# Performance work log

Measured on AMD Instinct MI355X. Metric: run time of the kernel, lower is better.

The kernel has to match this reference:

```python
import jax, jax.numpy as jnp
import numpy as np

RBF_START = 0.0
RBF_END = 12.0
RBF_STEPS = 32
ENERGY_SCALE = 0.01


def setup_inputs() -> dict:
    key = jax.random.key(0)
    k1, k2, k3, k4 = jax.random.split(key, 4)
    B, L, R, E, F = 8, 128, 2048, RBF_STEPS, 64
    return {
        "lig_feat": jax.random.normal(k1, (B, L, E, F), dtype=jnp.float32),
        "rec_feat": jax.random.normal(k2, (B, R, E, F), dtype=jnp.float32),
        "lig_coord": jax.random.normal(k3, (B, L, 3), dtype=jnp.float32),
        "rec_coord": jax.random.normal(k4, (B, R, 3), dtype=jnp.float32),
    }


def reference(lig_feat, rec_feat, lig_coord, rec_coord):
    # atn_coefs: contract feature dim f -> [B, L, R, E]
    atn_coefs = jnp.einsum('blef,bref->blre', lig_feat, rec_feat)
    # pairwise distances [B, L, R]
    diff = lig_coord[:, :, None, :] - rec_coord[:, None, :, :]
    dists = jnp.sqrt(jnp.sum(diff * diff, axis=-1))
    # RBF expansion [B, L, R, E]
    mu = jnp.linspace(RBF_START, RBF_END, RBF_STEPS, dtype=jnp.float32)
    sigma = (RBF_START - RBF_END) / RBF_STEPS
    z = (dists[..., None] - mu) / sigma
    rbfs = jnp.exp(-(z * z))
    # per-entry scalar energy [B]
    U = jnp.sum(atn_coefs * rbfs * ENERGY_SCALE, axis=(1, 2, 3))
    return U
```

## Files before the change

kernel.cpp:

```cpp
#include <hip/hip_runtime.h>
#include <hip/hip_bf16.h>

#define NB 8
#define NL 128
#define NR 2048
#define NE 32
#define NF 64
#define RT 128
#define NRT (NR / RT)
#define EH 4
#define EPB (NE / EH)
#define NTHREADS 512
#define NWAVES (NTHREADS / 64)

typedef __attribute__((ext_vector_type(4)))  float f32x4;
typedef __attribute__((ext_vector_type(16))) float f32x16;
typedef __attribute__((ext_vector_type(8)))  short s16x8;

__device__ __forceinline__ unsigned short f2bf(float x) {
    union { float f; unsigned u; } v; v.f = x;
    unsigned u = v.u;
    u += 0x7fffu + ((u >> 16) & 1u);
    return (unsigned short)(u >> 16);
}

__device__ __forceinline__ unsigned long long pack4(f32x4 v) {
    unsigned long long lo = (unsigned)f2bf(v.x) | ((unsigned)f2bf(v.y) << 16);
    unsigned long long hi = (unsigned)f2bf(v.z) | ((unsigned)f2bf(v.w) << 16);
    return lo | (hi << 32);
}

__global__ __launch_bounds__(NTHREADS, 4) void ff_kernel(
    const float* __restrict__ lig_feat,
    const float* __restrict__ rec_feat,
    const float* __restrict__ lig_coord,
    const float* __restrict__ rec_coord,
    float* __restrict__ out)
{
    __shared__ __align__(16) unsigned short sA[2][NL * NF];
    __shared__ __align__(16) unsigned short sB[2][RT * NF];
    __shared__ float sLc[3][NL];
    __shared__ float sRc[3][RT];
    __shared__ float sRed[NWAVES];

    const int blk = blockIdx.x;
    const int eh  = blk & (EH - 1);
    const int rt  = (blk >> 2) & (NRT - 1);
    const int b   = blk >> 6;
    const int e0  = eh * EPB;
    const int r0  = rt * RT;
    const int t   = threadIdx.x;
    const int lane = t & 63;
    const int wv   = t >> 6;

    for (int i = t; i < 3 * NL; i += NTHREADS) {
        const int c = i >> 7, l = i & 127;
        sLc[c][l] = lig_coord[((long)b * NL + l) * 3 + c];
    }
    for (int i = t; i < 3 * RT; i += NTHREADS) {
        const int c = i >> 7, r = i & 127;
        sRc[c][r] = rec_coord[((long)b * NR + r0 + r) * 3 + c];
    }

    f32x4 tA[4], tB[4];
    #pragma unroll
    for (int j = 0; j < 4; ++j) {
        const int idx = t + NTHREADS * j;
        const int f4 = idx & 15, l = idx >> 4;
        tA[j] = *(const f32x4*)(lig_feat + (((long)b * NL + l) * NE + e0) * NF + f4 * 4);
    }
    #pragma unroll
    for (int j = 0; j < 4; ++j) {
        const int idx = t + NTHREADS * j;
        const int f4 = idx & 15, r = idx >> 4;
        tB[j] = *(const f32x4*)(rec_feat + (((long)b * NR + r0 + r) * NE + e0) * NF + f4 * 4);
    }
    __syncthreads();

    const int n  = lane & 31;
    const int h  = lane >> 5;
    const int tr  = wv & 3;
    const int tl0 = wv >> 2;
    const int colr = tr * 32 + n;
    const float rx = sRc[0][colr], ry = sRc[1][colr], rz = sRc[2][colr];
    float d[2][16];
    #pragma unroll
    for (int t2 = 0; t2 < 2; ++t2) {
        const int tl = tl0 + 2 * t2;
        #pragma unroll
        for (int i = 0; i < 16; ++i) {
            const int row = tl * 32 + 4 * h + (i & 3) + ((i >> 2) << 3);
            const float dx = sLc[0][row] - rx;
            const float dy = sLc[1][row] - ry;
            const float dz = sLc[2][row] - rz;
            d[t2][i] = sqrtf(dx * dx + dy * dy + dz * dz);
        }
    }

    #pragma unroll
    for (int j = 0; j < 4; ++j) {
        const int idx = t + NTHREADS * j;
        const int f4 = idx & 15, l = idx >> 4;
        const int pos = (((f4 >> 1) ^ (l & 7)) << 3) + ((f4 & 1) << 2);
        *(unsigned long long*)&sA[0][l * NF + pos] = pack4(tA[j]);
    }
    #pragma unroll
    for (int j = 0; j < 4; ++j) {
        const int idx = t + NTHREADS * j;
        const int f4 = idx & 15, r = idx >> 4;
        const int pos = (((f4 >> 1) ^ (r & 7)) << 3) + ((f4 & 1) << 2);
        *(unsigned long long*)&sB[0][r * NF + pos] = pack4(tB[j]);
    }
    if (EPB > 1) {
        #pragma unroll
        for (int j = 0; j < 4; ++j) {
            const int idx = t + NTHREADS * j;
            const int f4 = idx & 15, l = idx >> 4;
            tA[j] = *(const f32x4*)(lig_feat + (((long)b * NL + l) * NE + e0 + 1) * NF + f4 * 4);
        }
        #pragma unroll
        for (int j = 0; j < 4; ++j) {
            const int idx = t + NTHREADS * j;
            const int f4 = idx & 15, r = idx >> 4;
            tB[j] = *(const f32x4*)(rec_feat + (((long)b * NR + r0 + r) * NE + e0 + 1) * NF + f4 * 4);
        }
    }
    __syncthreads();

    const float inv_s   = 32.0f / 12.0f;
    const float mu_step = 12.0f / 31.0f;
    const int sw = (n & 7);
    const int aBase = (tl0 * 32 + n) * NF;
    const int bBase = (tr * 32 + n) * NF;

    float sum = 0.0f;

    for (int ep = 0; ep < EPB; ++ep) {
        const int cur = ep & 1;

        if (ep + 1 < EPB) {
            #pragma unroll
            for (int j = 0; j < 4; ++j) {
                const int idx = t + NTHREADS * j;
                const int f4 = idx & 15, l = idx >> 4;
                const int pos = (((f4 >> 1) ^ (l & 7)) << 3) + ((f4 & 1) << 2);
                *(unsigned long long*)&sA[cur ^ 1][l * NF + pos] = pack4(tA[j]);
            }
            #pragma unroll
            for (int j = 0; j < 4; ++j) {
                const int idx = t + NTHREADS * j;
                const int f4 = idx & 15, r = idx >> 4;
                const int pos = (((f4 >> 1) ^ (r & 7)) << 3) + ((f4 & 1) << 2);
                *(unsigned long long*)&sB[cur ^ 1][r * NF + pos] = pack4(tB[j]);
            }
        }
        if (ep + 2 < EPB) {
            const int en = e0 + ep + 2;
            #pragma unroll
            for (int j = 0; j < 4; ++j) {
                const int idx = t + NTHREADS * j;
                const int f4 = idx & 15, l = idx >> 4;
                tA[j] = *(const f32x4*)(lig_feat + (((long)b * NL + l) * NE + en) * NF + f4 * 4);
            }
            #pragma unroll
            for (int j = 0; j < 4; ++j) {
                const int idx = t + NTHREADS * j;
                const int f4 = idx & 15, r = idx >> 4;
                tB[j] = *(const f32x4*)(rec_feat + (((long)b * NR + r0 + r) * NE + en) * NF + f4 * 4);
            }
        }

        const float mu = (float)(e0 + ep) * mu_step;
        #pragma unroll
        for (int t2 = 0; t2 < 2; ++t2) {
            const unsigned short* pa = &sA[cur][aBase + t2 * 64 * NF];
            const unsigned short* pb = &sB[cur][bBase];
            f32x16 acc = {0,0,0,0,0,0,0,0,0,0,0,0,0,0,0,0};
            #pragma unroll
            for (int kc = 0; kc < 4; ++kc) {
                const int ck = kc * 2 + h;
                const s16x8 af = *(const s16x8*)&pa[(ck ^ sw) << 3];
                const s16x8 bf = *(const s16x8*)&pb[(ck ^ sw) << 3];
                acc = __builtin_amdgcn_mfma_f32_32x32x16_bf16(af, bf, acc, 0, 0, 0);
            }
            #pragma unroll
            for (int i = 0; i < 16; ++i) {
                const float z = (d[t2][i] - mu) * inv_s;
                sum += __expf(-z * z) * acc[i];
            }
        }

        if (ep + 1 < EPB) __syncthreads();
    }

    sum *= 0.01f;
    #pragma unroll
    for (int off = 32; off > 0; off >>= 1)
        sum += __shfl_down(sum, off, 64);
    if (lane == 0) sRed[wv] = sum;
    __syncthreads();
    if (t == 0) {
        float s = 0.f;
        #pragma unroll
        for (int w = 0; w < NWAVES; ++w) s += sRed[w];
        atomicAdd(&out[b], s);
    }
}

extern "C" void kernel_launch(void* const* d_in, const int* in_sizes, int n_in,
                              void* d_out, int out_size, void* d_ws, size_t ws_size,
                              hipStream_t stream) {
    const float* lig_feat  = (const float*)d_in[0];
    const float* rec_feat  = (const float*)d_in[1];
    const float* lig_coord = (const float*)d_in[2];
    const float* rec_coord = (const float*)d_in[3];
    float* out = (float*)d_out;

    hipMemsetAsync(out, 0, (size_t)out_size * sizeof(float), stream);

    dim3 grid(NB * NRT * EH);
    ff_kernel<<<grid, NTHREADS, 0, stream>>>(lig_feat, rec_feat,
                                             lig_coord, rec_coord, out);
}
```

Before: 207.7 us.

## Use 2x2 MFMA tiles per wave with 256 threads and cheaper bf16 packing

Halves the block to 256 threads and gives each wave a 64x64 output tile computed as a 2x2 grid of 32x32 MFMAs, so every LDS fragment feeds two MFMAs instead of one. bf16 conversion now uses a single perm with round-half-up instead of round-to-nearest-even bit arithmetic, and the RBF argument becomes one fma with a precomputed negative mu. This cuts LDS read traffic and ALU work per MFMA, but raises register use (more staging registers and four accumulators), and the launch bound drops to 2 blocks, which may lower occupancy.

```diff
diff --git a/kernel.cpp b/kernel.cpp
--- a/kernel.cpp
+++ b/kernel.cpp
@@ -10,27 +10,27 @@
 #define NRT (NR / RT)
 #define EH 4
 #define EPB (NE / EH)
-#define NTHREADS 512
+#define NTHREADS 256
 #define NWAVES (NTHREADS / 64)
 
 typedef __attribute__((ext_vector_type(4)))  float f32x4;
 typedef __attribute__((ext_vector_type(16))) float f32x16;
 typedef __attribute__((ext_vector_type(8)))  short s16x8;
-
-__device__ __forceinline__ unsigned short f2bf(float x) {
-    union { float f; unsigned u; } v; v.f = x;
-    unsigned u = v.u;
-    u += 0x7fffu + ((u >> 16) & 1u);
-    return (unsigned short)(u >> 16);
-}
-
-__device__ __forceinline__ unsigned long long pack4(f32x4 v) {
-    unsigned long long lo = (unsigned)f2bf(v.x) | ((unsigned)f2bf(v.y) << 16);
-    unsigned long long hi = (unsigned)f2bf(v.z) | ((unsigned)f2bf(v.w) << 16);
-    return lo | (hi << 32);
-}
-
-__global__ __launch_bounds__(NTHREADS, 4) void ff_kernel(
+typedef __attribute__((ext_vector_type(2)))  unsigned int u32x2;
+
+__device__ __forceinline__ unsigned bf16pair(float a, float b) {
+    union { float f; unsigned u; } ua, ub; ua.f = a; ub.f = b;
+    return __builtin_amdgcn_perm(ub.u + 0x8000u, ua.u + 0x8000u, 0x07060302u);
+}
+
+__device__ __forceinline__ u32x2 pack4(f32x4 v) {
+    u32x2 r;
+    r.x = bf16pair(v.x, v.y);
+    r.y = bf16pair(v.z, v.w);
+    return r;
+}
+
+__global__ __launch_bounds__(NTHREADS, 2) void ff_kernel(
     const float* __restrict__ lig_feat,
     const float* __restrict__ rec_feat,
     const float* __restrict__ lig_coord,
@@ -62,15 +62,15 @@
         sRc[c][r] = rec_coord[((long)b * NR + r0 + r) * 3 + c];
     }
 
-    f32x4 tA[4], tB[4];
-    #pragma unroll
-    for (int j = 0; j < 4; ++j) {
+    f32x4 tA[8], tB[8];
+    #pragma unroll
+    for (int j = 0; j < 8; ++j) {
         const int idx = t + NTHREADS * j;
         const int f4 = idx & 15, l = idx >> 4;
         tA[j] = *(const f32x4*)(lig_feat + (((long)b * NL + l) * NE + e0) * NF + f4 * 4);
     }
     #pragma unroll
-    for (int j = 0; j < 4; ++j) {
+    for (int j = 0; j < 8; ++j) {
         const int idx = t + NTHREADS * j;
         const int f4 = idx & 15, r = idx >> 4;
         tB[j] = *(const f32x4*)(rec_feat + (((long)b * NR + r0 + r) * NE + e0) * NF + f4 * 4);
@@ -79,47 +79,49 @@
 
     const int n  = lane & 31;
     const int h  = lane >> 5;
-    const int tr  = wv & 3;
-    const int tl0 = wv >> 2;
-    const int colr = tr * 32 + n;
-    const float rx = sRc[0][colr], ry = sRc[1][colr], rz = sRc[2][colr];
-    float d[2][16];
-    #pragma unroll
-    for (int t2 = 0; t2 < 2; ++t2) {
-        const int tl = tl0 + 2 * t2;
-        #pragma unroll
-        for (int i = 0; i < 16; ++i) {
-            const int row = tl * 32 + 4 * h + (i & 3) + ((i >> 2) << 3);
-            const float dx = sLc[0][row] - rx;
-            const float dy = sLc[1][row] - ry;
-            const float dz = sLc[2][row] - rz;
-            d[t2][i] = sqrtf(dx * dx + dy * dy + dz * dz);
-        }
-    }
-
-    #pragma unroll
-    for (int j = 0; j < 4; ++j) {
+    const int wl = wv >> 1;
+    const int wr = wv & 1;
+    float d[2][2][16];
+    #pragma unroll
+    for (int j2 = 0; j2 < 2; ++j2) {
+        const int col = wr * 64 + j2 * 32 + n;
+        const float rx = sRc[0][col], ry = sRc[1][col], rz = sRc[2][col];
+        #pragma unroll
+        for (int i2 = 0; i2 < 2; ++i2) {
+            #pragma unroll
+            for (int i = 0; i < 16; ++i) {
+                const int row = wl * 64 + i2 * 32 + 4 * h + (i & 3) + ((i >> 2) << 3);
+                const float dx = sLc[0][row] - rx;
+                const float dy = sLc[1][row] - ry;
+                const float dz = sLc[2][row] - rz;
+                d[i2][j2][i] = sqrtf(dx * dx + dy * dy + dz * dz);
+            }
+        }
+    }
+
+    #pragma unroll
+    for (int j = 0; j < 8; ++j) {
         const int idx = t + NTHREADS * j;
         const int f4 = idx & 15, l = idx >> 4;
         const int pos = (((f4 >> 1) ^ (l & 7)) << 3) + ((f4 & 1) << 2);
-        *(unsigned long long*)&sA[0][l * NF + pos] = pack4(tA[j]);
-    }
-    #pragma unroll
-    for (int j = 0; j < 4; ++j) {
+        *(u32x2*)&sA[0][l * NF + pos] = pack4(tA[j]);
+    }
+    #pragma unroll
+    for (int j = 0; j < 8; ++j) {
         const int idx = t + NTHREADS * j;
         const int f4 = idx & 15, r = idx >> 4;
         const int pos = (((f4 >> 1) ^ (r & 7)) << 3) + ((f4 & 1) << 2);
-        *(unsigned long long*)&sB[0][r * NF + pos] = pack4(tB[j]);
+        *(u32x2*)&sB[0][r * NF + pos] = pack4(tB[j]);
     }
     if (EPB > 1) {
         #pragma unroll
-        for (int j = 0; j < 4; ++j) {
+        for (int j = 0; j < 8; ++j) {
             const int idx = t + NTHREADS * j;
             const int f4 = idx & 15, l = idx >> 4;
             tA[j] = *(const f32x4*)(lig_feat + (((long)b * NL + l) * NE + e0 + 1) * NF + f4 * 4);
         }
         #pragma unroll
-        for (int j = 0; j < 4; ++j) {
+        for (int j = 0; j < 8; ++j) {
             const int idx = t + NTHREADS * j;
             const int f4 = idx & 15, r = idx >> 4;
             tB[j] = *(const f32x4*)(rec_feat + (((long)b * NR + r0 + r) * NE + e0 + 1) * NF + f4 * 4);
@@ -128,10 +130,9 @@
     __syncthreads();
 
     const float inv_s   = 32.0f / 12.0f;
-    const float mu_step = 12.0f / 31.0f;
     const int sw = (n & 7);
-    const int aBase = (tl0 * 32 + n) * NF;
-    const int bBase = (tr * 32 + n) * NF;
+    const int aRow0 = (wl * 64 + n) * NF;
+    const int bRow0 = (wr * 64 + n) * NF;
 
     float sum = 0.0f;
 
@@ -140,54 +141,58 @@
 
         if (ep + 1 < EPB) {
             #pragma unroll
-            for (int j = 0; j < 4; ++j) {
+            for (int j = 0; j < 8; ++j) {
                 const int idx = t + NTHREADS * j;
                 const int f4 = idx & 15, l = idx >> 4;
                 const int pos = (((f4 >> 1) ^ (l & 7)) << 3) + ((f4 & 1) << 2);
-                *(unsigned long long*)&sA[cur ^ 1][l * NF + pos] = pack4(tA[j]);
-            }
-            #pragma unroll
-            for (int j = 0; j < 4; ++j) {
+                *(u32x2*)&sA[cur ^ 1][l * NF + pos] = pack4(tA[j]);
+            }
+            #pragma unroll
+            for (int j = 0; j < 8; ++j) {
                 const int idx = t + NTHREADS * j;
                 const int f4 = idx & 15, r = idx >> 4;
                 const int pos = (((f4 >> 1) ^ (r & 7)) << 3) + ((f4 & 1) << 2);
-                *(unsigned long long*)&sB[cur ^ 1][r * NF + pos] = pack4(tB[j]);
+                *(u32x2*)&sB[cur ^ 1][r * NF + pos] = pack4(tB[j]);
             }
         }
         if (ep + 2 < EPB) {
             const int en = e0 + ep + 2;
             #pragma unroll
-            for (int j = 0; j < 4; ++j) {
+            for (int j = 0; j < 8; ++j) {
                 const int idx = t + NTHREADS * j;
                 const int f4 = idx & 15, l = idx >> 4;
                 tA[j] = *(const f32x4*)(lig_feat + (((long)b * NL + l) * NE + en) * NF + f4 * 4);
             }
             #pragma unroll
-            for (int j = 0; j < 4; ++j) {
+            for (int j = 0; j < 8; ++j) {
                 const int idx = t + NTHREADS * j;
                 const int f4 = idx & 15, r = idx >> 4;
                 tB[j] = *(const f32x4*)(rec_feat + (((long)b * NR + r0 + r) * NE + en) * NF + f4 * 4);
             }
         }
 
-        const float mu = (float)(e0 + ep) * mu_step;
-        #pragma unroll
-        for (int t2 = 0; t2 < 2; ++t2) {
-            const unsigned short* pa = &sA[cur][aBase + t2 * 64 * NF];
-            const unsigned short* pb = &sB[cur][bBase];
-            f32x16 acc = {0,0,0,0,0,0,0,0,0,0,0,0,0,0,0,0};
-            #pragma unroll
-            for (int kc = 0; kc < 4; ++kc) {
-                const int ck = kc * 2 + h;
-                const s16x8 af = *(const s16x8*)&pa[(ck ^ sw) << 3];
-                const s16x8 bf = *(const s16x8*)&pb[(ck ^ sw) << 3];
-                acc = __builtin_amdgcn_mfma_f32_32x32x16_bf16(af, bf, acc, 0, 0, 0);
-            }
-            #pragma unroll
-            for (int i = 0; i < 16; ++i) {
-                const float z = (d[t2][i] - mu) * inv_s;
-                sum += __expf(-z * z) * acc[i];
-            }
+        f32x16 acc00 = {0,0,0,0,0,0,0,0,0,0,0,0,0,0,0,0};
+        f32x16 acc01 = acc00, acc10 = acc00, acc11 = acc00;
+        #pragma unroll
+        for (int kc = 0; kc < 4; ++kc) {
+            const int off = (((kc * 2 + h) ^ sw) << 3);
+            const s16x8 a0 = *(const s16x8*)&sA[cur][aRow0 + off];
+            const s16x8 a1 = *(const s16x8*)&sA[cur][aRow0 + 32 * NF + off];
+            const s16x8 b0 = *(const s16x8*)&sB[cur][bRow0 + off];
+            const s16x8 b1 = *(const s16x8*)&sB[cur][bRow0 + 32 * NF + off];
+            acc00 = __builtin_amdgcn_mfma_f32_32x32x16_bf16(a0, b0, acc00, 0, 0, 0);
+            acc01 = __builtin_amdgcn_mfma_f32_32x32x16_bf16(a0, b1, acc01, 0, 0, 0);
+            acc10 = __builtin_amdgcn_mfma_f32_32x32x16_bf16(a1, b0, acc10, 0, 0, 0);
+            acc11 = __builtin_amdgcn_mfma_f32_32x32x16_bf16(a1, b1, acc11, 0, 0, 0);
+        }
+        const float nmu = -(float)(e0 + ep) * (32.0f / 31.0f);
+        #pragma unroll
+        for (int i = 0; i < 16; ++i) {
+            float z;
+            z = __builtin_fmaf(d[0][0][i], inv_s, nmu); sum += __expf(-z * z) * acc00[i];
+            z = __builtin_fmaf(d[0][1][i], inv_s, nmu); sum += __expf(-z * z) * acc01[i];
+            z = __builtin_fmaf(d[1][0][i], inv_s, nmu); sum += __expf(-z * z) * acc10[i];
+            z = __builtin_fmaf(d[1][1][i], inv_s, nmu); sum += __expf(-z * z) * acc11[i];
         }
 
         if (ep + 1 < EPB) __syncthreads();
```

Result: slower. 223.2 us (+7.5%).

## Pipeline feature loads with inline-asm async loads and interleaved dual MFMA tiles

Applied to the files above, without the earlier changes.

Global feature loads become inline-asm global_load_dwordx4 with an explicit s_waitcnt placed after the MFMA and RBF work, so the prefetch for step ep+2 overlaps compute. The two MFMA accumulator chains are interleaved and share B-fragment loads. The bf16 pack uses a cheaper round-half-up conversion with v_perm, and the RBF argument is computed as a single fma. Launch bounds drop to 2 blocks per CU to allow more registers, which may reduce occupancy. The bf16 rounding no longer uses ties-to-even.

```diff
diff --git a/kernel.cpp b/kernel.cpp
--- a/kernel.cpp
+++ b/kernel.cpp
@@ -1,5 +1,4 @@
 #include <hip/hip_runtime.h>
-#include <hip/hip_bf16.h>
 
 #define NB 8
 #define NL 128
@@ -16,21 +15,25 @@
 typedef __attribute__((ext_vector_type(4)))  float f32x4;
 typedef __attribute__((ext_vector_type(16))) float f32x16;
 typedef __attribute__((ext_vector_type(8)))  short s16x8;
-
-__device__ __forceinline__ unsigned short f2bf(float x) {
-    union { float f; unsigned u; } v; v.f = x;
-    unsigned u = v.u;
-    u += 0x7fffu + ((u >> 16) & 1u);
-    return (unsigned short)(u >> 16);
-}
-
-__device__ __forceinline__ unsigned long long pack4(f32x4 v) {
-    unsigned long long lo = (unsigned)f2bf(v.x) | ((unsigned)f2bf(v.y) << 16);
-    unsigned long long hi = (unsigned)f2bf(v.z) | ((unsigned)f2bf(v.w) << 16);
-    return lo | (hi << 32);
-}
-
-__global__ __launch_bounds__(NTHREADS, 4) void ff_kernel(
+typedef __attribute__((ext_vector_type(2)))  unsigned int u32x2;
+
+__device__ __forceinline__ unsigned bf16pair(float a, float b) {
+    union { float f; unsigned u; } ua, ub; ua.f = a; ub.f = b;
+    return __builtin_amdgcn_perm(ub.u + 0x8000u, ua.u + 0x8000u, 0x07060302u);
+}
+
+__device__ __forceinline__ u32x2 pack4(f32x4 v) {
+    u32x2 r;
+    r.x = bf16pair(v.x, v.y);
+    r.y = bf16pair(v.z, v.w);
+    return r;
+}
+
+__device__ __forceinline__ void async_load4(f32x4& r, const float* p) {
+    asm volatile("global_load_dwordx4 %0, %1, off" : "=v"(r) : "v"(p) : "memory");
+}
+
+__global__ __launch_bounds__(NTHREADS, 2) void ff_kernel(
     const float* __restrict__ lig_feat,
     const float* __restrict__ rec_feat,
     const float* __restrict__ lig_coord,
@@ -53,6 +56,9 @@
     const int lane = t & 63;
     const int wv   = t >> 6;
 
+    const int f4    = t & 15;
+    const int row00 = t >> 4;
+
     for (int i = t; i < 3 * NL; i += NTHREADS) {
         const int c = i >> 7, l = i & 127;
         sLc[c][l] = lig_coord[((long)b * NL + l) * 3 + c];
@@ -64,17 +70,12 @@
 
     f32x4 tA[4], tB[4];
     #pragma unroll
-    for (int j = 0; j < 4; ++j) {
-        const int idx = t + NTHREADS * j;
-        const int f4 = idx & 15, l = idx >> 4;
-        tA[j] = *(const f32x4*)(lig_feat + (((long)b * NL + l) * NE + e0) * NF + f4 * 4);
-    }
-    #pragma unroll
-    for (int j = 0; j < 4; ++j) {
-        const int idx = t + NTHREADS * j;
-        const int f4 = idx & 15, r = idx >> 4;
-        tB[j] = *(const f32x4*)(rec_feat + (((long)b * NR + r0 + r) * NE + e0) * NF + f4 * 4);
-    }
+    for (int j = 0; j < 4; ++j)
+        tA[j] = *(const f32x4*)(lig_feat + (((long)b * NL + (row00 + 32 * j)) * NE + e0) * NF + f4 * 4);
+    #pragma unroll
+    for (int j = 0; j < 4; ++j)
+        tB[j] = *(const f32x4*)(rec_feat + (((long)b * NR + r0 + (row00 + 32 * j)) * NE + e0) * NF + f4 * 4);
+
     __syncthreads();
 
     const int n  = lane & 31;
@@ -99,98 +100,84 @@
 
     #pragma unroll
     for (int j = 0; j < 4; ++j) {
-        const int idx = t + NTHREADS * j;
-        const int f4 = idx & 15, l = idx >> 4;
-        const int pos = (((f4 >> 1) ^ (l & 7)) << 3) + ((f4 & 1) << 2);
-        *(unsigned long long*)&sA[0][l * NF + pos] = pack4(tA[j]);
+        const int r = row00 + 32 * j;
+        const int pos = (((f4 >> 1) ^ (r & 7)) << 3) + ((f4 & 1) << 2);
+        *(u32x2*)&sA[0][r * NF + pos] = pack4(tA[j]);
     }
     #pragma unroll
     for (int j = 0; j < 4; ++j) {
-        const int idx = t + NTHREADS * j;
-        const int f4 = idx & 15, r = idx >> 4;
+        const int r = row00 + 32 * j;
         const int pos = (((f4 >> 1) ^ (r & 7)) << 3) + ((f4 & 1) << 2);
-        *(unsigned long long*)&sB[0][r * NF + pos] = pack4(tB[j]);
+        *(u32x2*)&sB[0][r * NF + pos] = pack4(tB[j]);
     }
     if (EPB > 1) {
         #pragma unroll
-        for (int j = 0; j < 4; ++j) {
-            const int idx = t + NTHREADS * j;
-            const int f4 = idx & 15, l = idx >> 4;
-            tA[j] = *(const f32x4*)(lig_feat + (((long)b * NL + l) * NE + e0 + 1) * NF + f4 * 4);
-        }
-        #pragma unroll
-        for (int j = 0; j < 4; ++j) {
-            const int idx = t + NTHREADS * j;
-            const int f4 = idx & 15, r = idx >> 4;
-            tB[j] = *(const f32x4*)(rec_feat + (((long)b * NR + r0 + r) * NE + e0 + 1) * NF + f4 * 4);
-        }
+        for (int j = 0; j < 4; ++j)
+            async_load4(tA[j], lig_feat + (((long)b * NL + (row00 + 32 * j)) * NE + e0 + 1) * NF + f4 * 4);
+        #pragma unroll
+        for (int j = 0; j < 4; ++j)
+            async_load4(tB[j], rec_feat + (((long)b * NR + r0 + (row00 + 32 * j)) * NE + e0 + 1) * NF + f4 * 4);
     }
     __syncthreads();
 
-    const float inv_s   = 32.0f / 12.0f;
-    const float mu_step = 12.0f / 31.0f;
-    const int sw = (n & 7);
-    const int aBase = (tl0 * 32 + n) * NF;
-    const int bBase = (tr * 32 + n) * NF;
+    const float inv_s = 32.0f / 12.0f;
+    const int sw = n & 7;
+    const int aRow = (tl0 * 32 + n) * NF;
+    const int bRow = (tr * 32 + n) * NF;
 
     float sum = 0.0f;
 
+    #pragma unroll
     for (int ep = 0; ep < EPB; ++ep) {
         const int cur = ep & 1;
 
+        f32x16 acc0 = {0,0,0,0,0,0,0,0,0,0,0,0,0,0,0,0};
+        f32x16 acc1 = acc0;
+        #pragma unroll
+        for (int kc = 0; kc < 4; ++kc) {
+            const int off = (((kc * 2 + h) ^ sw) << 3);
+            const s16x8 a0 = *(const s16x8*)&sA[cur][aRow + off];
+            const s16x8 a1 = *(const s16x8*)&sA[cur][aRow + 64 * NF + off];
+            const s16x8 bf = *(const s16x8*)&sB[cur][bRow + off];
+            acc0 = __builtin_amdgcn_mfma_f32_32x32x16_bf16(a0, bf, acc0, 0, 0, 0);
+            acc1 = __builtin_amdgcn_mfma_f32_32x32x16_bf16(a1, bf, acc1, 0, 0, 0);
+        }
+        const float nmu = -(float)(e0 + ep) * (32.0f / 31.0f);
+        #pragma unroll
+        for (int i = 0; i < 16; ++i) {
+            float z;
+            z = __builtin_fmaf(d[0][i], inv_s, nmu); sum += __expf(-z * z) * acc0[i];
+            z = __builtin_fmaf(d[1][i], inv_s, nmu); sum += __expf(-z * z) * acc1[i];
+        }
+
         if (ep + 1 < EPB) {
+            asm volatile("s_waitcnt vmcnt(0)"
+                         : "+v"(tA[0]), "+v"(tA[1]), "+v"(tA[2]), "+v"(tA[3]),
+                           "+v"(tB[0]), "+v"(tB[1]), "+v"(tB[2]), "+v"(tB[3])
+                         :: "memory");
             #pragma unroll
             for (int j = 0; j < 4; ++j) {
-                const int idx = t + NTHREADS * j;
-                const int f4 = idx & 15, l = idx >> 4;
-                const int pos = (((f4 >> 1) ^ (l & 7)) << 3) + ((f4 & 1) << 2);
-                *(unsigned long long*)&sA[cur ^ 1][l * NF + pos] = pack4(tA[j]);
+                const int r = row00 + 32 * j;
+                const int pos = (((f4 >> 1) ^ (r & 7)) << 3) + ((f4 & 1) << 2);
+                *(u32x2*)&sA[cur ^ 1][r * NF + pos] = pack4(tA[j]);
             }
             #pragma unroll
             for (int j = 0; j < 4; ++j) {
-                const int idx = t + NTHREADS * j;
-                const int f4 = idx & 15, r = idx >> 4;
+                const int r = row00 + 32 * j;
                 const int pos = (((f4 >> 1) ^ (r & 7)) << 3) + ((f4 & 1) << 2);
-                *(unsigned long long*)&sB[cur ^ 1][r * NF + pos] = pack4(tB[j]);
+                *(u32x2*)&sB[cur ^ 1][r * NF + pos] = pack4(tB[j]);
             }
-        }
-        if (ep + 2 < EPB) {
-            const int en = e0 + ep + 2;
-            #pragma unroll
-            for (int j = 0; j < 4; ++j) {
-                const int idx = t + NTHREADS * j;
-                const int f4 = idx & 15, l = idx >> 4;
-                tA[j] = *(const f32x4*)(lig_feat + (((long)b * NL + l) * NE + en) * NF + f4 * 4);
+            if (ep + 2 < EPB) {
+                const int en = e0 + ep + 2;
+                #pragma unroll
+                for (int j = 0; j < 4; ++j)
+                    async_load4(tA[j], lig_feat + (((long)b * NL + (row00 + 32 * j)) * NE + en) * NF + f4 * 4);
+                #pragma unroll
+                for (int j = 0; j < 4; ++j)
+                    async_load4(tB[j], rec_feat + (((long)b * NR + r0 + (row00 + 32 * j)) * NE + en) * NF + f4 * 4);
             }
-            #pragma unroll
-            for (int j = 0; j < 4; ++j) {
-                const int idx = t + NTHREADS * j;
-                const int f4 = idx & 15, r = idx >> 4;
-                tB[j] = *(const f32x4*)(rec_feat + (((long)b * NR + r0 + r) * NE + en) * NF + f4 * 4);
-            }
-        }
-
-        const float mu = (float)(e0 + ep) * mu_step;
-        #pragma unroll
-        for (int t2 = 0; t2 < 2; ++t2) {
-            const unsigned short* pa = &sA[cur][aBase + t2 * 64 * NF];
-            const unsigned short* pb = &sB[cur][bBase];
-            f32x16 acc = {0,0,0,0,0,0,0,0,0,0,0,0,0,0,0,0};
-            #pragma unroll
-            for (int kc = 0; kc < 4; ++kc) {
-                const int ck = kc * 2 + h;
-                const s16x8 af = *(const s16x8*)&pa[(ck ^ sw) << 3];
-                const s16x8 bf = *(const s16x8*)&pb[(ck ^ sw) << 3];
-                acc = __builtin_amdgcn_mfma_f32_32x32x16_bf16(af, bf, acc, 0, 0, 0);
-            }
-            #pragma unroll
-            for (int i = 0; i < 16; ++i) {
-                const float z = (d[t2][i] - mu) * inv_s;
-                sum += __expf(-z * z) * acc[i];
-            }
-        }
-
-        if (ep + 1 < EPB) __syncthreads();
+            __syncthreads();
+        }
     }
 
     sum *= 0.01f;
```

New measurement: 207.1 us. About the same (-0.3%).
